# Performance work log

Hardware: AMD Instinct MI355X
Metric: run time of the kernel (lower is better)

The kernel has to match this reference:

```python
import jax, jax.numpy as jnp
import numpy as np

NUM_SEGMENTS = 8192  # number of graphs in the batch


def setup_inputs() -> dict:
    key = jax.random.key(0)
    ks = jax.random.split(key, 6)
    N, D, H, B = 1_000_000, 128, 512, NUM_SEGMENTS
    x_variables = jax.random.normal(ks[0], (N, D), dtype=jnp.float32)
    x_virtual_constraints = jax.random.normal(ks[1], (B, D), dtype=jnp.float32)
    x_variables_batch = jnp.sort(jax.random.randint(ks[2], (N,), 0, B))
    W1 = jax.random.normal(ks[3], (2 * D, H), dtype=jnp.float32) * (1.0 / np.sqrt(2 * D))
    b1 = jnp.zeros((H,), dtype=jnp.float32)
    W2 = jax.random.normal(ks[4], (H, D), dtype=jnp.float32) * (1.0 / np.sqrt(H))
    b2 = jnp.zeros((D,), dtype=jnp.float32)
    return {
        "x_variables": x_variables,
        "x_virtual_constraints": x_virtual_constraints,
        "x_variables_batch": x_variables_batch,
        "W1": W1, "b1": b1, "W2": W2, "b2": b2,
    }


def reference(x_variables, x_virtual_constraints, x_variables_batch, W1, b1, W2, b2):
    # scatter-mean over dim 0: segment_sum / counts (empty segments -> 0, as in torch_scatter mean)
    seg_sum = jax.ops.segment_sum(x_variables, x_variables_batch, num_segments=NUM_SEGMENTS)  # [B, D]
    counts = jax.ops.segment_sum(jnp.ones((x_variables.shape[0],), x_variables.dtype),
                                 x_variables_batch, num_segments=NUM_SEGMENTS)  # [B]
    x_mean = seg_sum / jnp.maximum(counts, 1.0)[:, None]
    x = jnp.concatenate([x_mean, x_virtual_constraints], axis=-1)  # [B, 2D]
    h = jax.nn.relu(x @ W1 + b1)
    return h @ W2 + b2
```

## Files before the change

### kernel.cpp

```cpp
#include <hip/hip_runtime.h>

#define DIM 128
#define HID 512
#define NSEG 8192
#define MLP_ROWS 16

__global__ __launch_bounds__(256) void boundaries_kernel(
    const int* __restrict__ batch, int* __restrict__ seg_start, int N, int B)
{
    int i = blockIdx.x * 256 + threadIdx.x;
    if (i >= N) return;
    int b = batch[i];
    if (i == 0) {
        for (int s = 0; s <= b; ++s) seg_start[s] = 0;
    } else {
        int p = batch[i - 1];
        for (int s = p + 1; s <= b; ++s) seg_start[s] = i;
    }
    if (i == N - 1) {
        for (int s = b + 1; s <= B; ++s) seg_start[s] = N;
    }
}

__global__ __launch_bounds__(256) void seg_mean_kernel(
    const float* __restrict__ x, const int* __restrict__ seg_start,
    float* __restrict__ xmean)
{
    __shared__ float4 part[8][32];
    const int s   = blockIdx.x;
    const int lo  = seg_start[s];
    const int hi  = seg_start[s + 1];
    const int tid = threadIdx.x;
    const int colg  = tid & 31;
    const int phase = tid >> 5;

    float4 a0 = make_float4(0.f, 0.f, 0.f, 0.f);
    float4 a1 = make_float4(0.f, 0.f, 0.f, 0.f);
    const float* base = x + (size_t)colg * 4;
    int r = lo + phase;
    for (; r + 8 < hi; r += 16) {
        const float4 v0 = *reinterpret_cast<const float4*>(base + (size_t)r * DIM);
        const float4 v1 = *reinterpret_cast<const float4*>(base + (size_t)(r + 8) * DIM);
        a0.x += v0.x; a0.y += v0.y; a0.z += v0.z; a0.w += v0.w;
        a1.x += v1.x; a1.y += v1.y; a1.z += v1.z; a1.w += v1.w;
    }
    if (r < hi) {
        const float4 v0 = *reinterpret_cast<const float4*>(base + (size_t)r * DIM);
        a0.x += v0.x; a0.y += v0.y; a0.z += v0.z; a0.w += v0.w;
    }
    a0.x += a1.x; a0.y += a1.y; a0.z += a1.z; a0.w += a1.w;
    part[phase][colg] = a0;
    __syncthreads();

    if (tid < 32) {
        float4 t = part[0][tid];
        #pragma unroll
        for (int p = 1; p < 8; ++p) {
            float4 u = part[p][tid];
            t.x += u.x; t.y += u.y; t.z += u.z; t.w += u.w;
        }
        const float inv = (hi > lo) ? 1.0f / (float)(hi - lo) : 0.0f;
        t.x *= inv; t.y *= inv; t.z *= inv; t.w *= inv;
        *reinterpret_cast<float4*>(xmean + (size_t)s * DIM + tid * 4) = t;
    }
}

__global__ __launch_bounds__(256) void mlp_kernel(
    const float* __restrict__ xmean, const float* __restrict__ xvc,
    const float* __restrict__ W1, const float* __restrict__ b1,
    const float* __restrict__ W2, const float* __restrict__ b2,
    float* __restrict__ out)
{
    __shared__ float Xs[MLP_ROWS][2 * DIM];
    __shared__ float Hs[MLP_ROWS][HID];
    const int tid  = threadIdx.x;
    const int row0 = blockIdx.x * MLP_ROWS;

    #pragma unroll
    for (int i = 0; i < 4; ++i) {
        const int flat = tid + 256 * i;
        const int r    = flat >> 6;
        const int cg   = flat & 63;
        const float4 v = (cg < 32)
            ? *reinterpret_cast<const float4*>(xmean + (size_t)(row0 + r) * DIM + cg * 4)
            : *reinterpret_cast<const float4*>(xvc   + (size_t)(row0 + r) * DIM + (cg - 32) * 4);
        *reinterpret_cast<float4*>(&Xs[r][cg * 4]) = v;
    }
    __syncthreads();

    {
        const int cg = tid & 127;
        const int c0 = cg << 2;
        const int rb = (tid >> 7) << 3;
        float acc[8][4];
        {
            const float4 bb = *reinterpret_cast<const float4*>(b1 + c0);
            #pragma unroll
            for (int r = 0; r < 8; ++r) {
                acc[r][0] = bb.x; acc[r][1] = bb.y; acc[r][2] = bb.z; acc[r][3] = bb.w;
            }
        }
        for (int k = 0; k < 2 * DIM; k += 4) {
            float w[4][4];
            #pragma unroll
            for (int kk = 0; kk < 4; ++kk)
                *reinterpret_cast<float4*>(w[kk]) =
                    *reinterpret_cast<const float4*>(W1 + (size_t)(k + kk) * HID + c0);
            #pragma unroll
            for (int r = 0; r < 8; ++r) {
                float xr[4];
                *reinterpret_cast<float4*>(xr) =
                    *reinterpret_cast<const float4*>(&Xs[rb + r][k]);
                #pragma unroll
                for (int kk = 0; kk < 4; ++kk)
                    #pragma unroll
                    for (int j = 0; j < 4; ++j)
                        acc[r][j] = fmaf(xr[kk], w[kk][j], acc[r][j]);
            }
        }
        #pragma unroll
        for (int r = 0; r < 8; ++r) {
            float4 h;
            h.x = fmaxf(acc[r][0], 0.f); h.y = fmaxf(acc[r][1], 0.f);
            h.z = fmaxf(acc[r][2], 0.f); h.w = fmaxf(acc[r][3], 0.f);
            *reinterpret_cast<float4*>(&Hs[rb + r][c0]) = h;
        }
    }
    __syncthreads();

    {
        const int cg = tid & 31;
        const int c0 = cg << 2;
        const int rb = (tid >> 5) << 1;
        float acc[2][4];
        {
            const float4 bb = *reinterpret_cast<const float4*>(b2 + c0);
            #pragma unroll
            for (int r = 0; r < 2; ++r) {
                acc[r][0] = bb.x; acc[r][1] = bb.y; acc[r][2] = bb.z; acc[r][3] = bb.w;
            }
        }
        for (int k = 0; k < HID; k += 4) {
            float w[4][4];
            #pragma unroll
            for (int kk = 0; kk < 4; ++kk)
                *reinterpret_cast<float4*>(w[kk]) =
                    *reinterpret_cast<const float4*>(W2 + (size_t)(k + kk) * DIM + c0);
            #pragma unroll
            for (int r = 0; r < 2; ++r) {
                float h[4];
                *reinterpret_cast<float4*>(h) =
                    *reinterpret_cast<const float4*>(&Hs[rb + r][k]);
                #pragma unroll
                for (int kk = 0; kk < 4; ++kk)
                    #pragma unroll
                    for (int j = 0; j < 4; ++j)
                        acc[r][j] = fmaf(h[kk], w[kk][j], acc[r][j]);
            }
        }
        #pragma unroll
        for (int r = 0; r < 2; ++r) {
            *reinterpret_cast<float4*>(out + (size_t)(row0 + rb + r) * DIM + c0) =
                make_float4(acc[r][0], acc[r][1], acc[r][2], acc[r][3]);
        }
    }
}

extern "C" void kernel_launch(void* const* d_in, const int* in_sizes, int n_in,
                              void* d_out, int out_size, void* d_ws, size_t ws_size,
                              hipStream_t stream) {
    const float* x     = (const float*)d_in[0];
    const float* xvc   = (const float*)d_in[1];
    const int*   batch = (const int*)d_in[2];
    const float* W1    = (const float*)d_in[3];
    const float* b1    = (const float*)d_in[4];
    const float* W2    = (const float*)d_in[5];
    const float* b2    = (const float*)d_in[6];
    float*       out   = (float*)d_out;

    const int N = in_sizes[2];
    const int B = in_sizes[1] / DIM;

    float* xmean    = (float*)d_ws;
    int*   segstart = (int*)((char*)d_ws + (size_t)B * DIM * sizeof(float));

    boundaries_kernel<<<(N + 255) / 256, 256, 0, stream>>>(batch, segstart, N, B);
    seg_mean_kernel<<<B, 256, 0, stream>>>(x, segstart, xmean);
    mlp_kernel<<<B / MLP_ROWS, 256, 0, stream>>>(xmean, xvc, W1, b1, W2, b2, out);
}
```

Before: 740.2 us.

## Fuse boundary search, segment mean and MLP into one kernel

Replaces the three-kernel pipeline (boundary scan, per-segment mean, MLP) with one kernel. Each block handles 16 segments: it binary-searches the sorted batch array for segment bounds, reduces the rows of each segment into shared memory with a 4-way unrolled loop, then runs the two-layer MLP directly from shared memory. This drops two launches, the boundary kernel and the global xmean round trip. In exchange, the bandwidth-heavy reduction now runs on only B/16 blocks that walk their segments one after another with barriers in between, which cuts memory-level parallelism compared with one block per segment.

```diff
diff --git a/kernel.cpp b/kernel.cpp
--- a/kernel.cpp
+++ b/kernel.cpp
@@ -1,92 +1,80 @@
 #include <hip/hip_runtime.h>
+
 
 #define DIM 128
 #define HID 512
-#define NSEG 8192
-#define MLP_ROWS 16
+#define SEGS 16
 
-__global__ __launch_bounds__(256) void boundaries_kernel(
-    const int* __restrict__ batch, int* __restrict__ seg_start, int N, int B)
-{
-    int i = blockIdx.x * 256 + threadIdx.x;
-    if (i >= N) return;
-    int b = batch[i];
-    if (i == 0) {
-        for (int s = 0; s <= b; ++s) seg_start[s] = 0;
-    } else {
-        int p = batch[i - 1];
-        for (int s = p + 1; s <= b; ++s) seg_start[s] = i;
-    }
-    if (i == N - 1) {
-        for (int s = b + 1; s <= B; ++s) seg_start[s] = N;
-    }
+__device__ __forceinline__ void f4add(float4& a, const float4 b) {
+    a.x += b.x; a.y += b.y; a.z += b.z; a.w += b.w;
 }
 
-__global__ __launch_bounds__(256) void seg_mean_kernel(
-    const float* __restrict__ x, const int* __restrict__ seg_start,
-    float* __restrict__ xmean)
+__global__ __launch_bounds__(256) void fused_virtual_aggr(
+    const float* __restrict__ x, const float* __restrict__ xvc,
+    const int* __restrict__ batch,
+    const float* __restrict__ W1, const float* __restrict__ b1,
+    const float* __restrict__ W2, const float* __restrict__ b2,
+    float* __restrict__ out, int N)
 {
+    __shared__ float Xs[SEGS][2 * DIM];
+    __shared__ float Hs[SEGS][HID];
     __shared__ float4 part[8][32];
-    const int s   = blockIdx.x;
-    const int lo  = seg_start[s];
-    const int hi  = seg_start[s + 1];
+    __shared__ int bound[SEGS + 1];
+
     const int tid = threadIdx.x;
+    const int s0  = blockIdx.x * SEGS;
+
+    if (tid <= SEGS) {
+        const int s = s0 + tid;
+        int lo = 0, hi = N;
+        while (lo < hi) {
+            const int mid = (lo + hi) >> 1;
+            if (batch[mid] < s) lo = mid + 1; else hi = mid;
+        }
+        bound[tid] = lo;
+    }
+
+    #pragma unroll
+    for (int i = 0; i < 2; ++i) {
+        const int flat = tid + 256 * i;
+        const int r  = flat >> 5;
+        const int cg = flat & 31;
+        *reinterpret_cast<float4*>(&Xs[r][DIM + cg * 4]) =
+            *reinterpret_cast<const float4*>(xvc + (size_t)(s0 + r) * DIM + cg * 4);
+    }
+    __syncthreads();
+
     const int colg  = tid & 31;
     const int phase = tid >> 5;
-
-    float4 a0 = make_float4(0.f, 0.f, 0.f, 0.f);
-    float4 a1 = make_float4(0.f, 0.f, 0.f, 0.f);
-    const float* base = x + (size_t)colg * 4;
-    int r = lo + phase;
-    for (; r + 8 < hi; r += 16) {
-        const float4 v0 = *reinterpret_cast<const float4*>(base + (size_t)r * DIM);
-        const float4 v1 = *reinterpret_cast<const float4*>(base + (size_t)(r + 8) * DIM);
-        a0.x += v0.x; a0.y += v0.y; a0.z += v0.z; a0.w += v0.w;
-        a1.x += v1.x; a1.y += v1.y; a1.z += v1.z; a1.w += v1.w;
+    const float* basecol = x + colg * 4;
+    for (int j = 0; j < SEGS; ++j) {
+        const int lo = bound[j], hi = bound[j + 1];
+        float4 a0 = {0,0,0,0}, a1 = {0,0,0,0}, a2 = {0,0,0,0}, a3 = {0,0,0,0};
+        int r = lo + phase;
+        for (; r + 24 < hi; r += 32) {
+            const float4 v0 = *reinterpret_cast<const float4*>(basecol + (size_t)r * DIM);
+            const float4 v1 = *reinterpret_cast<const float4*>(basecol + (size_t)(r + 8) * DIM);
+            const float4 v2 = *reinterpret_cast<const float4*>(basecol + (size_t)(r + 16) * DIM);
+            const float4 v3 = *reinterpret_cast<const float4*>(basecol + (size_t)(r + 24) * DIM);
+            f4add(a0, v0); f4add(a1, v1); f4add(a2, v2); f4add(a3, v3);
+        }
+        for (; r < hi; r += 8) {
+            const float4 v = *reinterpret_cast<const float4*>(basecol + (size_t)r * DIM);
+            f4add(a0, v);
+        }
+        f4add(a0, a1); f4add(a2, a3); f4add(a0, a2);
+        part[phase][colg] = a0;
+        __syncthreads();
+        if (tid < 32) {
+            float4 t = part[0][tid];
+            #pragma unroll
+            for (int p = 1; p < 8; ++p) f4add(t, part[p][tid]);
+            const float inv = (hi > lo) ? 1.0f / (float)(hi - lo) : 0.0f;
+            t.x *= inv; t.y *= inv; t.z *= inv; t.w *= inv;
+            *reinterpret_cast<float4*>(&Xs[j][tid * 4]) = t;
+        }
+        __syncthreads();
     }
-    if (r < hi) {
-        const float4 v0 = *reinterpret_cast<const float4*>(base + (size_t)r * DIM);
-        a0.x += v0.x; a0.y += v0.y; a0.z += v0.z; a0.w += v0.w;
-    }
-    a0.x += a1.x; a0.y += a1.y; a0.z += a1.z; a0.w += a1.w;
-    part[phase][colg] = a0;
-    __syncthreads();
-
-    if (tid < 32) {
-        float4 t = part[0][tid];
-        #pragma unroll
-        for (int p = 1; p < 8; ++p) {
-            float4 u = part[p][tid];
-            t.x += u.x; t.y += u.y; t.z += u.z; t.w += u.w;
-        }
-        const float inv = (hi > lo) ? 1.0f / (float)(hi - lo) : 0.0f;
-        t.x *= inv; t.y *= inv; t.z *= inv; t.w *= inv;
-        *reinterpret_cast<float4*>(xmean + (size_t)s * DIM + tid * 4) = t;
-    }
-}
-
-__global__ __launch_bounds__(256) void mlp_kernel(
-    const float* __restrict__ xmean, const float* __restrict__ xvc,
-    const float* __restrict__ W1, const float* __restrict__ b1,
-    const float* __restrict__ W2, const float* __restrict__ b2,
-    float* __restrict__ out)
-{
-    __shared__ float Xs[MLP_ROWS][2 * DIM];
-    __shared__ float Hs[MLP_ROWS][HID];
-    const int tid  = threadIdx.x;
-    const int row0 = blockIdx.x * MLP_ROWS;
-
-    #pragma unroll
-    for (int i = 0; i < 4; ++i) {
-        const int flat = tid + 256 * i;
-        const int r    = flat >> 6;
-        const int cg   = flat & 63;
-        const float4 v = (cg < 32)
-            ? *reinterpret_cast<const float4*>(xmean + (size_t)(row0 + r) * DIM + cg * 4)
-            : *reinterpret_cast<const float4*>(xvc   + (size_t)(row0 + r) * DIM + (cg - 32) * 4);
-        *reinterpret_cast<float4*>(&Xs[r][cg * 4]) = v;
-    }
-    __syncthreads();
 
     {
         const int cg = tid & 127;
@@ -160,7 +148,7 @@
         }
         #pragma unroll
         for (int r = 0; r < 2; ++r) {
-            *reinterpret_cast<float4*>(out + (size_t)(row0 + rb + r) * DIM + c0) =
+            *reinterpret_cast<float4*>(out + (size_t)(s0 + rb + r) * DIM + c0) =
                 make_float4(acc[r][0], acc[r][1], acc[r][2], acc[r][3]);
         }
     }
@@ -181,10 +169,6 @@
     const int N = in_sizes[2];
     const int B = in_sizes[1] / DIM;
 
-    float* xmean    = (float*)d_ws;
-    int*   segstart = (int*)((char*)d_ws + (size_t)B * DIM * sizeof(float));
-
-    boundaries_kernel<<<(N + 255) / 256, 256, 0, stream>>>(batch, segstart, N, B);
-    seg_mean_kernel<<<B, 256, 0, stream>>>(x, segstart, xmean);
-    mlp_kernel<<<B / MLP_ROWS, 256, 0, stream>>>(xmean, xvc, W1, b1, W2, b2, out);
+    fused_virtual_aggr<<<B / SEGS, 256, 0, stream>>>(
+        x, xvc, batch, W1, b1, W2, b2, out, N);
 }
```

Result: no change. 731.3 us (-1.2%).
